# Kernel tuning notes

Measured on AMD Instinct MI355X. Metric: run time of the kernel, lower is better.

The kernel has to match this reference:

```python
import jax, jax.numpy as jnp
import numpy as np
from functools import partial

C = 256
N_HEADS = 8
OFFSET_RANGE = 2.0


def _dwconv(x, w):
    # depthwise conv, SAME padding; w: (C,1,k,k)
    c = x.shape[1]
    return jax.lax.conv_general_dilated(
        x, w, window_strides=(1, 1), padding='SAME',
        feature_group_count=c, dimension_numbers=('NCHW', 'OIHW', 'NCHW'))


def _grid_sample_bilinear(x, gx, gy):
    # x: (B,C,H,W); gx,gy: (B,H,W) normalized in [-1,1]; align_corners=True
    B, Cc, H, W = x.shape
    ix = (gx + 1.0) * 0.5 * (W - 1)
    iy = (gy + 1.0) * 0.5 * (H - 1)
    x0f = jnp.floor(ix)
    y0f = jnp.floor(iy)
    fx = (ix - x0f)[:, None, :, :].reshape(B, 1, H * W)
    fy = (iy - y0f)[:, None, :, :].reshape(B, 1, H * W)
    x0 = jnp.clip(x0f.astype(jnp.int32), 0, W - 1)
    x1 = jnp.clip(x0 + 1, 0, W - 1)
    y0 = jnp.clip(y0f.astype(jnp.int32), 0, H - 1)
    y1 = jnp.clip(y0 + 1, 0, H - 1)
    xf = x.reshape(B, Cc, H * W)

    def gather(yi, xi):
        idx = (yi * W + xi).reshape(B, H * W)
        return jax.vmap(lambda f, i: f[:, i])(xf, idx)  # (B,C,N)

    v00 = gather(y0, x0)
    v01 = gather(y0, x1)
    v10 = gather(y1, x0)
    v11 = gather(y1, x1)
    out = (v00 * (1 - fx) * (1 - fy) + v01 * fx * (1 - fy)
           + v10 * (1 - fx) * fy + v11 * fx * fy)
    return out.reshape(B, Cc, H, W)


def setup_inputs() -> dict:
    key = jax.random.key(0)
    ks = jax.random.split(key, 11)
    B, H, W = 1, 64, 64
    s = 0.05
    return {
        'x': jax.random.normal(ks[0], (B, C, H, W), jnp.float32),
        'offset_weights': jnp.ones((3,), jnp.float32) + 0.1 * jax.random.normal(ks[1], (3,)),
        'w3': s * jax.random.normal(ks[2], (C, 1, 3, 3), jnp.float32),
        'w5': s * jax.random.normal(ks[3], (C, 1, 5, 5), jnp.float32),
        'w7': s * jax.random.normal(ks[4], (C, 1, 7, 7), jnp.float32),
        'w_offproj': s * jax.random.normal(ks[5], (2, C), jnp.float32),
        'wq': s * jax.random.normal(ks[6], (C, C), jnp.float32),
        'wk': s * jax.random.normal(ks[7], (C, C), jnp.float32),
        'wv': s * jax.random.normal(ks[8], (C, C), jnp.float32),
        'wo': s * jax.random.normal(ks[9], (C, C), jnp.float32),
        'beta': jnp.asarray(0.5, jnp.float32),
    }


def reference(x, offset_weights, w3, w5, w7, w_offproj, wq, wk, wv, wo, beta):
    B, Cc, H, W = x.shape
    head_dim = Cc // N_HEADS
    scale = head_dim ** -0.5
    N = H * W

    # multi-scale depthwise offset features
    off_feat = (_dwconv(x, w3) * offset_weights[0]
                + _dwconv(x, w5) * offset_weights[1]
                + _dwconv(x, w7) * offset_weights[2])
    offset = jnp.einsum('oc,bchw->bohw', w_offproj, jax.nn.relu(off_feat))  # (B,2,H,W) = (y,x)

    # reference points: ((i+0.5)/(size-1))*2 - 1
    ref_y = ((jnp.arange(H, dtype=jnp.float32) + 0.5) / (H - 1.0)) * 2.0 - 1.0
    ref_x = ((jnp.arange(W, dtype=jnp.float32) + 0.5) / (W - 1.0)) * 2.0 - 1.0
    gy = jnp.clip(ref_y[None, :, None] + jnp.tanh(offset[:, 0]) * OFFSET_RANGE, -1.0, 1.0)
    gx = jnp.clip(ref_x[None, None, :] + jnp.tanh(offset[:, 1]) * OFFSET_RANGE, -1.0, 1.0)
    x_sampled = _grid_sample_bilinear(x, gx, gy)

    # Manhattan decay bias
    yy = jnp.repeat(jnp.arange(H), W)
    xx = jnp.tile(jnp.arange(W), H)
    dist = (jnp.abs(yy[:, None] - yy[None, :]) + jnp.abs(xx[:, None] - xx[None, :])).astype(jnp.float32)
    decay = jnp.exp(-dist / (jnp.abs(beta) + 1e-6))  # (N,N)

    q = jnp.einsum('oc,bchw->bohw', wq, x).reshape(B, N_HEADS, head_dim, N)
    k = jnp.einsum('oc,bchw->bohw', wk, x_sampled).reshape(B, N_HEADS, head_dim, N)
    v = jnp.einsum('oc,bchw->bohw', wv, x_sampled).reshape(B, N_HEADS, head_dim, N)

    attn = jnp.einsum('bhdn,bhdm->bhnm', q, k) * scale + decay[None, None]
    attn = jax.nn.softmax(attn, axis=-1)
    out = jnp.einsum('bhnm,bhdm->bhdn', attn, v).reshape(B, Cc, H, W)
    return jnp.einsum('oc,bchw->bohw', wo, out)
```

## Files before the change

### kernel.cpp

```cpp
#include <hip/hip_runtime.h>
#include <hip/hip_bf16.h>


typedef __bf16 bf16x8 __attribute__((ext_vector_type(8)));
typedef float f32x4 __attribute__((ext_vector_type(4)));

__device__ __forceinline__ f32x4 mfma16(bf16x8 a, bf16x8 b, f32x4 c) {
    return __builtin_amdgcn_mfma_f32_16x16x32_bf16(a, b, c, 0, 0, 0);
}

__device__ __forceinline__ unsigned pack_bf16(float pa, float pb) {
    return __builtin_amdgcn_perm(__float_as_uint(pb), __float_as_uint(pa), 0x07060302u);
}

__device__ __forceinline__ float fast_tanh(float x) {
    const float t = __builtin_amdgcn_exp2f(x * 2.8853900817779268f);
    return (t - 1.0f) * __builtin_amdgcn_rcpf(t + 1.0f);
}

__global__ void prep_transpose_kernel(const float* __restrict__ x, float* __restrict__ xTf,
                                      __hip_bfloat16* __restrict__ xTb,
                                      const float* __restrict__ w3, const float* __restrict__ w5,
                                      const float* __restrict__ w7, const float* __restrict__ ow,
                                      const float* __restrict__ wq, const float* __restrict__ wk,
                                      const float* __restrict__ wv, const float* __restrict__ wo,
                                      float* __restrict__ wcomb, __hip_bfloat16* __restrict__ wb) {
    __shared__ float tile[32][33];
    const int b = blockIdx.x;
    if (b < 1024) {
        const int p0 = (b >> 3) * 32, c0 = (b & 7) * 32;
        const int tx = threadIdx.x & 31, ty = threadIdx.x >> 5;
#pragma unroll
        for (int i = 0; i < 4; ++i)
            tile[ty + i * 8][tx] = x[(size_t)(c0 + ty + i * 8) * 4096 + p0 + tx];
        __syncthreads();
#pragma unroll
        for (int i = 0; i < 4; ++i) {
            const float v = tile[tx][ty + i * 8];
            const size_t o = (size_t)(p0 + ty + i * 8) * 256 + c0 + tx;
            xTf[o] = v;
            xTb[o] = __float2bfloat16(v);
        }
    } else if (b < 1073) {
        const int i = b - 1024, c = threadIdx.x;
        const int dy = i / 7, dx = i % 7;
        float val = ow[2] * w7[c * 49 + i];
        if (dy >= 1 && dy <= 5 && dx >= 1 && dx <= 5)
            val += ow[1] * w5[c * 25 + (dy - 1) * 5 + (dx - 1)];
        if (dy >= 2 && dy <= 4 && dx >= 2 && dx <= 4)
            val += ow[0] * w3[c * 9 + (dy - 2) * 3 + (dx - 2)];
        wcomb[i * 256 + c] = val;
    } else {
        const int idx = (b - 1073) * 256 + threadIdx.x;
        const int m = idx >> 16;
        const float* src = (m == 0) ? wq : (m == 1) ? wk : (m == 2) ? wv : wo;
        const float sc = (m == 0) ? 0.25507535f : 1.0f;
        wb[idx] = __float2bfloat16(src[idx & 65535] * sc);
    }
}

__global__ __launch_bounds__(256) void sample_kernel(
    const float* __restrict__ xTf, const float* __restrict__ wcomb,
    const float* __restrict__ wop, __hip_bfloat16* __restrict__ xsT) {
    const int b = blockIdx.x;
    const int y = b >> 3;
    const int x0 = (b & 7) * 8;
    const int c = threadIdx.x;

    float wc[49];
#pragma unroll
    for (int i = 0; i < 49; ++i) wc[i] = wcomb[i * 256 + c];

    float acc[8];
#pragma unroll
    for (int px = 0; px < 8; ++px) acc[px] = 0.f;

#pragma unroll
    for (int dy = 0; dy < 7; ++dy) {
        const int yy = y + dy - 3;
        if (yy < 0 || yy > 63) continue;
        float v[14];
#pragma unroll
        for (int j = 0; j < 14; ++j) {
            const int xx = x0 - 3 + j;
            v[j] = (xx >= 0 && xx <= 63) ? xTf[(size_t)(yy * 64 + xx) * 256 + c] : 0.f;
        }
#pragma unroll
        for (int px = 0; px < 8; ++px)
#pragma unroll
            for (int dx = 0; dx < 7; ++dx)
                acc[px] = fmaf(v[px + dx], wc[dy * 7 + dx], acc[px]);
    }

    const float wy = wop[c], wx = wop[256 + c];
    float s[16];
#pragma unroll
    for (int px = 0; px < 8; ++px) {
        const float r = fmaxf(acc[px], 0.f);
        s[px] = wy * r;
        s[8 + px] = wx * r;
    }
#pragma unroll
    for (int off = 1; off < 64; off <<= 1)
#pragma unroll
        for (int i = 0; i < 16; ++i) s[i] += __shfl_xor(s[i], off, 64);

    __shared__ float red[4][16];
    const int lane = c & 63, wid = c >> 6;
    if (lane == 0)
#pragma unroll
        for (int i = 0; i < 16; ++i) red[wid][i] = s[i];
    __syncthreads();

#pragma unroll
    for (int px = 0; px < 8; ++px) {
        const float offy = red[0][px] + red[1][px] + red[2][px] + red[3][px];
        const float offx = red[0][8 + px] + red[1][8 + px] + red[2][8 + px] + red[3][8 + px];
        const int pxa = x0 + px;
        const float refy = ((y + 0.5f) / 63.0f) * 2.0f - 1.0f;
        const float refx = ((pxa + 0.5f) / 63.0f) * 2.0f - 1.0f;
        const float gy = fminf(fmaxf(refy + fast_tanh(offy) * 2.0f, -1.0f), 1.0f);
        const float gx = fminf(fmaxf(refx + fast_tanh(offx) * 2.0f, -1.0f), 1.0f);
        const float iy = (gy + 1.0f) * 31.5f;
        const float ix = (gx + 1.0f) * 31.5f;
        const float y0f = floorf(iy), x0f = floorf(ix);
        const float fy = iy - y0f, fx = ix - x0f;
        int yi0 = min(max((int)y0f, 0), 63), xi0 = min(max((int)x0f, 0), 63);
        int yi1 = min(yi0 + 1, 63), xi1 = min(xi0 + 1, 63);
        const float v00 = xTf[(size_t)(yi0 * 64 + xi0) * 256 + c];
        const float v01 = xTf[(size_t)(yi0 * 64 + xi1) * 256 + c];
        const float v10 = xTf[(size_t)(yi1 * 64 + xi0) * 256 + c];
        const float v11 = xTf[(size_t)(yi1 * 64 + xi1) * 256 + c];
        const float out = v00 * (1.f - fx) * (1.f - fy) + v01 * fx * (1.f - fy) +
                          v10 * (1.f - fx) * fy + v11 * fx * fy;
        xsT[(size_t)(y * 64 + pxa) * 256 + c] = __float2bfloat16(out);
    }
}

template <typename OutT>
__device__ __forceinline__ void gemm_body(const __hip_bfloat16* A, const __hip_bfloat16* B,
                                          OutT* out, int ldc, int m0, int n0) {
    const int w = threadIdx.x >> 6, lane = threadIdx.x & 63;
    const int g = lane >> 4, c = lane & 15;
    f32x4 acc[4];
#pragma unroll
    for (int nt = 0; nt < 4; ++nt) acc[nt] = (f32x4){0.f, 0.f, 0.f, 0.f};
    const __hip_bfloat16* Ar = A + (size_t)(m0 + w * 16 + c) * 256 + g * 8;
#pragma unroll
    for (int kc = 0; kc < 8; ++kc) {
        const bf16x8 a = *reinterpret_cast<const bf16x8*>(Ar + kc * 32);
#pragma unroll
        for (int nt = 0; nt < 4; ++nt) {
            const bf16x8 b = *reinterpret_cast<const bf16x8*>(
                B + (size_t)(n0 + nt * 16 + c) * 256 + kc * 32 + g * 8);
            acc[nt] = mfma16(a, b, acc[nt]);
        }
    }
#pragma unroll
    for (int nt = 0; nt < 4; ++nt)
#pragma unroll
        for (int r = 0; r < 4; ++r) {
            const size_t o = (size_t)(m0 + w * 16 + 4 * g + r) * ldc + n0 + nt * 16 + c;
            if constexpr (__is_same(OutT, float)) out[o] = acc[nt][r];
            else out[o] = __float2bfloat16(acc[nt][r]);
        }
}

__global__ __launch_bounds__(256) void gemm_qkv(const __hip_bfloat16* __restrict__ xq,
                                                const __hip_bfloat16* __restrict__ xs,
                                                const __hip_bfloat16* __restrict__ wb,
                                                __hip_bfloat16* __restrict__ q_t,
                                                __hip_bfloat16* __restrict__ k_t,
                                                __hip_bfloat16* __restrict__ vv) {
    const int z = blockIdx.z;
    if (z == 0)
        gemm_body<__hip_bfloat16>(xq, wb, q_t, 256, blockIdx.x * 64, blockIdx.y * 64);
    else if (z == 1)
        gemm_body<__hip_bfloat16>(xs, wb + 65536, k_t, 256, blockIdx.x * 64, blockIdx.y * 64);
    else
        gemm_body<__hip_bfloat16>(wb + 2 * 65536, xs, vv, 4096, blockIdx.y * 64,
                                  blockIdx.x * 64);
}

template <typename OutT>
__global__ __launch_bounds__(256) void gemm_abt(const __hip_bfloat16* __restrict__ A,
                                                const __hip_bfloat16* __restrict__ B,
                                                OutT* __restrict__ out, int ldc) {
    gemm_body<OutT>(A, B, out, ldc, blockIdx.x * 64, blockIdx.y * 64);
}

__global__ __launch_bounds__(256, 2) void attn_kernel(
    const __hip_bfloat16* __restrict__ q_t,
    const __hip_bfloat16* __restrict__ k_t,
    const __hip_bfloat16* __restrict__ vv,
    const float* __restrict__ beta_p,
    __hip_bfloat16* __restrict__ att)
{
    __shared__ __align__(16) char smem[37888];
    const int h = blockIdx.y;
    const int nb = blockIdx.x;
    const int n0 = nb * 64;
    const int tid = threadIdx.x;
    const int w = tid >> 6, lane = tid & 63, g = lane >> 4, c = lane & 15;

    const float bta = fabsf(beta_p[0]) + 1e-6f;
    const float L2E = 1.4426950408889634f;
    const float c2 = L2E / bta;

    float d64d[7][4];
#pragma unroll
    for (int dlt = 0; dlt < 7; ++dlt)
#pragma unroll
        for (int r = 0; r < 4; ++r) {
            const int dd = 16 * (dlt - 3) + c - 4 * g - r;
            d64d[dlt][r] = L2E * __builtin_amdgcn_exp2f(-c2 * fabsf((float)dd));
        }

    bf16x8 aq[4];
#pragma unroll
    for (int nt = 0; nt < 4; ++nt)
        aq[nt] = *reinterpret_cast<const bf16x8*>(
            q_t + (size_t)(n0 + nt * 16 + c) * 256 + h * 32 + g * 8);

    f32x4 o_acc[4][2];
    float l_part[4] = {0.f, 0.f, 0.f, 0.f};
#pragma unroll
    for (int nt = 0; nt < 4; ++nt) {
        o_acc[nt][0] = (f32x4){0.f, 0.f, 0.f, 0.f};
        o_acc[nt][1] = (f32x4){0.f, 0.f, 0.f, 0.f};
    }

    uint2* pl = (uint2*)smem + w * 1024;
    const int wbi = g * 16 + c;
    const int rb = (g >> 1) * 64 + (g & 1) * 32 + c;
    const f32x4 zf = (f32x4){0.f, 0.f, 0.f, 0.f};

    auto loadK = [&](int it, bf16x8* bk) {
        const size_t m0 = (size_t)(it * 4 + w) * 64;
#pragma unroll
        for (int mt = 0; mt < 4; ++mt)
            bk[mt] = *reinterpret_cast<const bf16x8*>(
                k_t + (m0 + mt * 16 + c) * 256 + h * 32 + g * 8);
    };
    auto loadV = [&](int it, bf16x8 (*bv)[2]) {
        const size_t m0 = (size_t)(it * 4 + w) * 64;
#pragma unroll
        for (int dt = 0; dt < 2; ++dt)
#pragma unroll
            for (int mc = 0; mc < 2; ++mc)
                bv[dt][mc] = *reinterpret_cast<const bf16x8*>(
                    vv + (size_t)(h * 32 + dt * 16 + c) * 4096 + m0 + mc * 32 + g * 8);
    };
    auto body = [&](int it, bf16x8* bk, bf16x8 (*bv)[2]) {
        const int ym = it * 4 + w;
        const float a2 = __builtin_amdgcn_exp2f(-c2 * fabsf((float)(nb - ym)));
#pragma unroll
        for (int nt = 0; nt < 4; ++nt) {
            f32x4 s[4];
#pragma unroll
            for (int mt = 0; mt < 4; ++mt) s[mt] = mfma16(bk[mt], aq[nt], zf);
#pragma unroll
            for (int mt = 0; mt < 4; ++mt) {
                float p[4];
#pragma unroll
                for (int r = 0; r < 4; ++r)
                    p[r] = __builtin_amdgcn_exp2f(fmaf(a2, d64d[nt - mt + 3][r], s[mt][r]));
                l_part[nt] += (p[0] + p[1]) + (p[2] + p[3]);
                pl[wbi + (nt * 4 + mt) * 64] = uint2{pack_bf16(p[0], p[1]),
                                                     pack_bf16(p[2], p[3])};
            }
        }
#pragma unroll
        for (int nt = 0; nt < 4; ++nt)
#pragma unroll
            for (int mc = 0; mc < 2; ++mc) {
                const int idx = rb + (nt * 4 + 2 * mc) * 64;
                union { uint2 u[2]; bf16x8 v; } t;
                t.u[0] = pl[idx];
                t.u[1] = pl[idx + 16];
                o_acc[nt][0] = mfma16(t.v, bv[0][mc], o_acc[nt][0]);
                o_acc[nt][1] = mfma16(t.v, bv[1][mc], o_acc[nt][1]);
            }
    };

    bf16x8 bkA[4], bkB[4], bvA[2][2], bvB[2][2];
    loadK(0, bkA);
    loadV(0, bvA);
#pragma unroll 1
    for (int it2 = 0; it2 < 8; ++it2) {
        loadK(2 * it2 + 1, bkB);
        loadV(2 * it2 + 1, bvB);
        body(2 * it2, bkA, bvA);
        if (it2 < 7) {
            loadK(2 * it2 + 2, bkA);
            loadV(2 * it2 + 2, bvA);
        }
        body(2 * it2 + 1, bkB, bvB);
    }

#pragma unroll
    for (int nt = 0; nt < 4; ++nt) {
        float v = l_part[nt];
        v += __shfl_xor(v, 16);
        v += __shfl_xor(v, 32);
        l_part[nt] = v;
    }

    __syncthreads();
    float* ob = (float*)smem;
    float* lred = (float*)(smem + 36864);
#pragma unroll
    for (int nt = 0; nt < 4; ++nt) {
        if (g == 0) lred[w * 64 + nt * 16 + c] = l_part[nt];
#pragma unroll
        for (int r = 0; r < 4; ++r) {
            const int row = 16 * nt + 4 * g + r;
            ob[w * 2304 + row * 36 + c] = o_acc[nt][0][r];
            ob[w * 2304 + row * 36 + 16 + c] = o_acc[nt][1][r];
        }
    }
    __syncthreads();

#pragma unroll
    for (int k = 0; k < 8; ++k) {
        const int flat = k * 256 + tid;
        const int row = flat >> 5, d = flat & 31;
        const float O = ob[row * 36 + d] + ob[2304 + row * 36 + d] +
                        ob[4608 + row * 36 + d] + ob[6912 + row * 36 + d];
        const float L = lred[row] + lred[64 + row] + lred[128 + row] + lred[192 + row];
        att[(size_t)(n0 + row) * 256 + h * 32 + d] = __float2bfloat16(O / L);
    }
}

extern "C" void kernel_launch(void* const* d_in, const int* in_sizes, int n_in,
                              void* d_out, int out_size, void* d_ws, size_t ws_size,
                              hipStream_t stream) {
    (void)in_sizes; (void)n_in; (void)out_size; (void)ws_size;
    const float* x    = (const float*)d_in[0];
    const float* ow   = (const float*)d_in[1];
    const float* w3   = (const float*)d_in[2];
    const float* w5   = (const float*)d_in[3];
    const float* w7   = (const float*)d_in[4];
    const float* wop  = (const float*)d_in[5];
    const float* wq   = (const float*)d_in[6];
    const float* wk   = (const float*)d_in[7];
    const float* wv   = (const float*)d_in[8];
    const float* wo   = (const float*)d_in[9];
    const float* beta = (const float*)d_in[10];

    char* ws = (char*)d_ws;
    const size_t MB = 1 << 20;
    float*          xTf = (float*)(ws);
    __hip_bfloat16* xTb = (__hip_bfloat16*)(ws + 4 * MB);
    __hip_bfloat16* xsT = (__hip_bfloat16*)(ws + 6 * MB);
    __hip_bfloat16* q_t = (__hip_bfloat16*)(ws + 8 * MB);
    __hip_bfloat16* k_t = (__hip_bfloat16*)(ws + 10 * MB);
    __hip_bfloat16* vv  = (__hip_bfloat16*)(ws + 12 * MB);
    __hip_bfloat16* att = (__hip_bfloat16*)(ws + 14 * MB);
    __hip_bfloat16* wb  = (__hip_bfloat16*)(ws + 16 * MB);
    float* wcomb        = (float*)(ws + 16 * MB + 512 * 1024);
    __hip_bfloat16* wob = wb + 3 * 65536;

    prep_transpose_kernel<<<2097, 256, 0, stream>>>(x, xTf, xTb, w3, w5, w7, ow,
                                                    wq, wk, wv, wo, wcomb, wb);
    sample_kernel<<<512, 256, 0, stream>>>(xTf, wcomb, wop, xsT);
    gemm_qkv<<<dim3(64, 4, 3), 256, 0, stream>>>(xTb, xsT, wb, q_t, k_t, vv);
    attn_kernel<<<dim3(64, 8), 256, 0, stream>>>(q_t, k_t, vv, beta, att);
    gemm_abt<float><<<dim3(4, 64), 256, 0, stream>>>(wob, att, (float*)d_out, 4096);
}
```

Before: 147.1 us.

## Split attention key range across two blocks and merge partials in output GEMM

The attention kernel now splits the 4096 keys into two halves, launching 128x8 blocks instead of 64x8, and writes unnormalized fp32 partial outputs and row sums to workspace. A new output-projection GEMM sums the two partials, normalizes by the combined sum, converts to bf16 on the fly and multiplies by Wo. This doubles the attention grid to better fill the CUs on a 512-block launch. In exchange it adds fp32 partial traffic (about 8 MB written and then read) and more global loads per MFMA in the final GEMM. Merging works without a running max only because the softmax is computed without max subtraction.

After: 168.4 us. 1.14x slower.

```diff
diff --git a/kernel.cpp b/kernel.cpp
--- a/kernel.cpp
+++ b/kernel.cpp
@@ -182,23 +182,19 @@
                                   blockIdx.x * 64);
 }
 
-template <typename OutT>
-__global__ __launch_bounds__(256) void gemm_abt(const __hip_bfloat16* __restrict__ A,
-                                                const __hip_bfloat16* __restrict__ B,
-                                                OutT* __restrict__ out, int ldc) {
-    gemm_body<OutT>(A, B, out, ldc, blockIdx.x * 64, blockIdx.y * 64);
-}
-
 __global__ __launch_bounds__(256, 2) void attn_kernel(
     const __hip_bfloat16* __restrict__ q_t,
     const __hip_bfloat16* __restrict__ k_t,
     const __hip_bfloat16* __restrict__ vv,
     const float* __restrict__ beta_p,
-    __hip_bfloat16* __restrict__ att)
+    float* __restrict__ opart,
+    float* __restrict__ lpart)
 {
     __shared__ __align__(16) char smem[37888];
     const int h = blockIdx.y;
-    const int nb = blockIdx.x;
+    const int nb2 = blockIdx.x;
+    const int nb = nb2 >> 1;
+    const int half = nb2 & 1;
     const int n0 = nb * 64;
     const int tid = threadIdx.x;
     const int w = tid >> 6, lane = tid & 63, g = lane >> 4, c = lane & 15;
@@ -236,14 +232,14 @@
     const f32x4 zf = (f32x4){0.f, 0.f, 0.f, 0.f};
 
     auto loadK = [&](int it, bf16x8* bk) {
-        const size_t m0 = (size_t)(it * 4 + w) * 64;
+        const size_t m0 = (size_t)(half * 32 + it * 4 + w) * 64;
 #pragma unroll
         for (int mt = 0; mt < 4; ++mt)
             bk[mt] = *reinterpret_cast<const bf16x8*>(
                 k_t + (m0 + mt * 16 + c) * 256 + h * 32 + g * 8);
     };
     auto loadV = [&](int it, bf16x8 (*bv)[2]) {
-        const size_t m0 = (size_t)(it * 4 + w) * 64;
+        const size_t m0 = (size_t)(half * 32 + it * 4 + w) * 64;
 #pragma unroll
         for (int dt = 0; dt < 2; ++dt)
 #pragma unroll
@@ -252,7 +248,7 @@
                     vv + (size_t)(h * 32 + dt * 16 + c) * 4096 + m0 + mc * 32 + g * 8);
     };
     auto body = [&](int it, bf16x8* bk, bf16x8 (*bv)[2]) {
-        const int ym = it * 4 + w;
+        const int ym = half * 32 + it * 4 + w;
         const float a2 = __builtin_amdgcn_exp2f(-c2 * fabsf((float)(nb - ym)));
 #pragma unroll
         for (int nt = 0; nt < 4; ++nt) {
@@ -287,11 +283,11 @@
     loadK(0, bkA);
     loadV(0, bvA);
 #pragma unroll 1
-    for (int it2 = 0; it2 < 8; ++it2) {
+    for (int it2 = 0; it2 < 4; ++it2) {
         loadK(2 * it2 + 1, bkB);
         loadV(2 * it2 + 1, bvB);
         body(2 * it2, bkA, bvA);
-        if (it2 < 7) {
+        if (it2 < 3) {
             loadK(2 * it2 + 2, bkA);
             loadV(2 * it2 + 2, bvA);
         }
@@ -327,9 +323,55 @@
         const int row = flat >> 5, d = flat & 31;
         const float O = ob[row * 36 + d] + ob[2304 + row * 36 + d] +
                         ob[4608 + row * 36 + d] + ob[6912 + row * 36 + d];
-        const float L = lred[row] + lred[64 + row] + lred[128 + row] + lred[192 + row];
-        att[(size_t)(n0 + row) * 256 + h * 32 + d] = __float2bfloat16(O / L);
-    }
+        opart[((size_t)half * 4096 + n0 + row) * 256 + h * 32 + d] = O;
+        if (d == 0) {
+            const float L = lred[row] + lred[64 + row] + lred[128 + row] + lred[192 + row];
+            lpart[(size_t)(half * 8 + h) * 4096 + n0 + row] = L;
+        }
+    }
+}
+
+__global__ __launch_bounds__(256) void gemm_out(const __hip_bfloat16* __restrict__ wob,
+                                                const float* __restrict__ opart,
+                                                const float* __restrict__ lpart,
+                                                float* __restrict__ out) {
+    const int m0 = blockIdx.x * 64, n0 = blockIdx.y * 64;
+    const int w = threadIdx.x >> 6, lane = threadIdx.x & 63;
+    const int g = lane >> 4, c = lane & 15;
+    f32x4 acc[4];
+#pragma unroll
+    for (int nt = 0; nt < 4; ++nt) acc[nt] = (f32x4){0.f, 0.f, 0.f, 0.f};
+    const __hip_bfloat16* Ar = wob + (size_t)(m0 + w * 16 + c) * 256 + g * 8;
+#pragma unroll
+    for (int kc = 0; kc < 8; ++kc) {
+        const bf16x8 a = *reinterpret_cast<const bf16x8*>(Ar + kc * 32);
+#pragma unroll
+        for (int nt = 0; nt < 4; ++nt) {
+            const int n = n0 + nt * 16 + c;
+            const float Linv = __builtin_amdgcn_rcpf(
+                lpart[(size_t)kc * 4096 + n] + lpart[(size_t)(8 + kc) * 4096 + n]);
+            const float4 p0a = *reinterpret_cast<const float4*>(
+                opart + (size_t)n * 256 + kc * 32 + g * 8);
+            const float4 p0b = *reinterpret_cast<const float4*>(
+                opart + (size_t)n * 256 + kc * 32 + g * 8 + 4);
+            const float4 p1a = *reinterpret_cast<const float4*>(
+                opart + (size_t)(4096 + n) * 256 + kc * 32 + g * 8);
+            const float4 p1b = *reinterpret_cast<const float4*>(
+                opart + (size_t)(4096 + n) * 256 + kc * 32 + g * 8 + 4);
+            bf16x8 b;
+#pragma unroll
+            for (int i = 0; i < 4; ++i) {
+                b[i] = (__bf16)((p0a[i] + p1a[i]) * Linv);
+                b[4 + i] = (__bf16)((p0b[i] + p1b[i]) * Linv);
+            }
+            acc[nt] = mfma16(a, b, acc[nt]);
+        }
+    }
+#pragma unroll
+    for (int nt = 0; nt < 4; ++nt)
+#pragma unroll
+        for (int r = 0; r < 4; ++r)
+            out[(size_t)(m0 + w * 16 + 4 * g + r) * 4096 + n0 + nt * 16 + c] = acc[nt][r];
 }
 
 extern "C" void kernel_launch(void* const* d_in, const int* in_sizes, int n_in,
@@ -350,21 +392,22 @@
 
     char* ws = (char*)d_ws;
     const size_t MB = 1 << 20;
-    float*          xTf = (float*)(ws);
-    __hip_bfloat16* xTb = (__hip_bfloat16*)(ws + 4 * MB);
-    __hip_bfloat16* xsT = (__hip_bfloat16*)(ws + 6 * MB);
-    __hip_bfloat16* q_t = (__hip_bfloat16*)(ws + 8 * MB);
-    __hip_bfloat16* k_t = (__hip_bfloat16*)(ws + 10 * MB);
-    __hip_bfloat16* vv  = (__hip_bfloat16*)(ws + 12 * MB);
-    __hip_bfloat16* att = (__hip_bfloat16*)(ws + 14 * MB);
-    __hip_bfloat16* wb  = (__hip_bfloat16*)(ws + 16 * MB);
-    float* wcomb        = (float*)(ws + 16 * MB + 512 * 1024);
-    __hip_bfloat16* wob = wb + 3 * 65536;
+    float*          xTf   = (float*)(ws);
+    __hip_bfloat16* xTb   = (__hip_bfloat16*)(ws + 4 * MB);
+    __hip_bfloat16* xsT   = (__hip_bfloat16*)(ws + 6 * MB);
+    __hip_bfloat16* q_t   = (__hip_bfloat16*)(ws + 8 * MB);
+    __hip_bfloat16* k_t   = (__hip_bfloat16*)(ws + 10 * MB);
+    __hip_bfloat16* vv    = (__hip_bfloat16*)(ws + 12 * MB);
+    float*          opart = (float*)(ws + 14 * MB);
+    float*          lpart = (float*)(ws + 22 * MB);
+    __hip_bfloat16* wb    = (__hip_bfloat16*)(ws + 23 * MB);
+    float* wcomb          = (float*)(ws + 23 * MB + 512 * 1024);
+    __hip_bfloat16* wob   = wb + 3 * 65536;
 
     prep_transpose_kernel<<<2097, 256, 0, stream>>>(x, xTf, xTb, w3, w5, w7, ow,
                                                     wq, wk, wv, wo, wcomb, wb);
     sample_kernel<<<512, 256, 0, stream>>>(xTf, wcomb, wop, xsT);
     gemm_qkv<<<dim3(64, 4, 3), 256, 0, stream>>>(xTb, xsT, wb, q_t, k_t, vv);
-    attn_kernel<<<dim3(64, 8), 256, 0, stream>>>(q_t, k_t, vv, beta, att);
-    gemm_abt<float><<<dim3(4, 64), 256, 0, stream>>>(wob, att, (float*)d_out, 4096);
-}
+    attn_kernel<<<dim3(128, 8), 256, 0, stream>>>(q_t, k_t, vv, beta, opart, lpart);
+    gemm_out<<<dim3(4, 64), 256, 0, stream>>>(wob, opart, lpart, (float*)d_out);
+}
```
